# Kernel optimization log

Hardware: AMD Instinct MI355X
Metric: run time of the kernel (lower is better)

## Reference

```python
import jax, jax.numpy as jnp
import numpy as np

B, S, D = 2, 2048, 1024
H = 16
HD = D // H  # 64
EPS = 1e-5


def setup_inputs() -> dict:
    key = jax.random.key(0)
    ks = jax.random.split(key, 9)
    s = 1.0 / np.sqrt(D)
    return {
        "x": jax.random.normal(ks[0], (B, S, D), jnp.float32),
        "Wq": jax.random.normal(ks[1], (D, D), jnp.float32) * s,
        "bq": jnp.zeros((D,), jnp.float32),
        "Wk": jax.random.normal(ks[2], (D, D), jnp.float32) * s,
        "bk": jnp.zeros((D,), jnp.float32),
        "Wv": jax.random.normal(ks[3], (D, D), jnp.float32) * s,
        "bv": jnp.zeros((D,), jnp.float32),
        "Wp": jax.random.normal(ks[4], (D, D), jnp.float32) * s,
        "bp": jnp.zeros((D,), jnp.float32),
        "gamma": jnp.ones((D,), jnp.float32),
        "beta": jnp.zeros((D,), jnp.float32),
    }


def reference(x, Wq, bq, Wk, bk, Wv, bv, Wp, bp, gamma, beta):
    # QKV projections -> [B, H, S, HD]
    def split_heads(t):
        return t.reshape(B, S, H, HD).transpose(0, 2, 1, 3)

    q = split_heads(x @ Wq + bq)
    k = split_heads(x @ Wk + bk)
    v = split_heads(x @ Wv + bv)

    scores = jnp.einsum('bhqd,bhkd->bhqk', q, k) / np.sqrt(HD).astype(jnp.float32)
    attn = jax.nn.softmax(scores, axis=-1)  # dropout in eval mode = identity
    out = jnp.einsum('bhqk,bhkd->bhqd', attn, v)
    out = out.transpose(0, 2, 1, 3).reshape(B, S, D)
    out = out @ Wp + bp  # dropout identity

    # residual + LayerNorm over last dim
    y = x + out
    mu = jnp.mean(y, axis=-1, keepdims=True)
    var = jnp.mean((y - mu) ** 2, axis=-1, keepdims=True)
    return (y - mu) / jnp.sqrt(var + EPS) * gamma + beta
```

## Files before the change

kernel.cpp:

```cpp
#include <hip/hip_runtime.h>

#define DI __device__ __forceinline__

typedef __bf16 bf16;
typedef __bf16 bf16x8 __attribute__((ext_vector_type(8)));
typedef __bf16 bf16x4 __attribute__((ext_vector_type(4)));
typedef float  f32x4  __attribute__((ext_vector_type(4)));

DI void async_copy16(const void* g, void* s) {
  __builtin_amdgcn_global_load_lds(
      (__attribute__((address_space(1))) unsigned int*)(void*)g,
      (__attribute__((address_space(3))) unsigned int*)s,
      16, 0, 0);
}

DI f32x4 mfma16(bf16x8 a, bf16x8 b, f32x4 c) {
  return __builtin_amdgcn_mfma_f32_16x16x32_bf16(a, b, c, 0, 0, 0);
}


__global__ __launch_bounds__(256) void convert_x(const float* __restrict__ x,
                                                 bf16* __restrict__ xb) {
  int t = blockIdx.x * 256 + threadIdx.x;
  float4 v = ((const float4*)x)[t];
  bf16x4 o;
  o[0] = (bf16)v.x; o[1] = (bf16)v.y; o[2] = (bf16)v.z; o[3] = (bf16)v.w;
  *(bf16x4*)&xb[t * 4] = o;
}

__global__ __launch_bounds__(256) void transpose_w(const float* __restrict__ Wq,
                                                   const float* __restrict__ Wk,
                                                   const float* __restrict__ Wv,
                                                   const float* __restrict__ Wp,
                                                   bf16* __restrict__ Wt) {
  __shared__ float tile[32][33];
  const float* W = (blockIdx.z == 0) ? Wq : (blockIdx.z == 1) ? Wk
                 : (blockIdx.z == 2) ? Wv : Wp;
  int n0 = blockIdx.x * 32, k0 = blockIdx.y * 32;
  int tx = threadIdx.x, ty = threadIdx.y;
#pragma unroll
  for (int i = 0; i < 4; ++i)
    tile[ty + i * 8][tx] = W[(k0 + ty + i * 8) * 1024 + n0 + tx];
  __syncthreads();
#pragma unroll
  for (int i = 0; i < 4; ++i)
    Wt[((int)blockIdx.z * 1024 + n0 + ty + i * 8) * 1024 + k0 + tx] =
        (bf16)tile[tx][ty + i * 8];
}

template <int MODE, int MT, int NT>
__global__ __launch_bounds__(256, 3) void gemm_bt(
    const bf16* __restrict__ A, const bf16* __restrict__ Bt,
    const float* __restrict__ bias0, const float* __restrict__ bias1,
    const float* __restrict__ bias2, bf16* __restrict__ Qo,
    bf16* __restrict__ Ko, bf16* __restrict__ Vo, float* __restrict__ Po) {
  constexpr int MW = MT / 2, NW = NT / 2;
  constexpr int MI = MW / 16, NI = NW / 16;
  const int tid = threadIdx.x;
  const int w = tid >> 6, lane = tid & 63, quad = lane >> 4, m16 = lane & 15;
  const int m0 = blockIdx.x * MT, n0 = blockIdx.y * NT;
  const int mw = (w >> 1) * MW, nw = (w & 1) * NW;
  const int sw = m16 & 7;

  __shared__ __align__(16) bf16 As[MT * 64];
  __shared__ __align__(16) bf16 Bs[NT * 64];

  f32x4 acc[MI][NI];
#pragma unroll
  for (int i = 0; i < MI; ++i)
#pragma unroll
    for (int j = 0; j < NI; ++j)
#pragma unroll
      for (int r = 0; r < 4; ++r) acc[i][j][r] = 0.0f;

  for (int k0 = 0; k0 < 1024; k0 += 64) {
    __syncthreads();
#pragma unroll
    for (int i = 0; i < MT / 32; ++i) {
      int lin = i * 256 + tid;
      int row = lin >> 3, p = lin & 7;
      async_copy16(&A[(m0 + row) * 1024 + k0 + ((p ^ (row & 7)) << 3)],
                   &As[(i * 256 + w * 64) * 8]);
    }
#pragma unroll
    for (int i = 0; i < NT / 32; ++i) {
      int lin = i * 256 + tid;
      int row = lin >> 3, p = lin & 7;
      async_copy16(&Bt[(n0 + row) * 1024 + k0 + ((p ^ (row & 7)) << 3)],
                   &Bs[(i * 256 + w * 64) * 8]);
    }
    __syncthreads();

#pragma unroll
    for (int kk = 0; kk < 2; ++kk) {
      const int pos = ((kk * 4 + quad) ^ sw) << 3;
      bf16x8 af[MI], bg[NI];
#pragma unroll
      for (int i = 0; i < MI; ++i)
        af[i] = *(const bf16x8*)&As[(mw + i * 16 + m16) * 64 + pos];
#pragma unroll
      for (int j = 0; j < NI; ++j)
        bg[j] = *(const bf16x8*)&Bs[(nw + j * 16 + m16) * 64 + pos];
#pragma unroll
      for (int i = 0; i < MI; ++i)
#pragma unroll
        for (int j = 0; j < NI; ++j) acc[i][j] = mfma16(af[i], bg[j], acc[i][j]);
    }
  }

  const float SC = 0.18033688011112042f;
#pragma unroll
  for (int i = 0; i < MI; ++i) {
#pragma unroll
    for (int j = 0; j < NI; ++j) {
      int np = n0 + nw + j * 16 + m16;
      if (MODE == 0) {
        int which = np >> 10, n = np & 1023;
        float bias = (which == 0) ? bias0[n] : (which == 1) ? bias1[n] : bias2[n];
        int h = n >> 6, hd = n & 63;
        if (which == 2) {
          bf16x4 pv;
          int m = m0 + mw + i * 16 + quad * 4;
          int b = m >> 11, s = m & 2047;
#pragma unroll
          for (int r = 0; r < 4; ++r) pv[r] = (bf16)(acc[i][j][r] + bias);
          *(bf16x4*)&Vo[((b * 16 + h) * 64 + hd) * 2048 + s] = pv;
        } else {
#pragma unroll
          for (int r = 0; r < 4; ++r) {
            int m = m0 + mw + i * 16 + quad * 4 + r;
            int b = m >> 11, s = m & 2047;
            float v = acc[i][j][r] + bias;
            if (which == 0)
              Qo[((b * 16 + h) * 2048 + s) * 64 + hd] = (bf16)(v * SC);
            else
              Ko[((b * 16 + h) * 2048 + s) * 64 + hd] = (bf16)v;
          }
        }
      } else {
        float bias = bias0[np];
#pragma unroll
        for (int r = 0; r < 4; ++r) {
          int m = m0 + mw + i * 16 + quad * 4 + r;
          Po[m * 1024 + np] = acc[i][j][r] + bias;
        }
      }
    }
  }
}

__global__ __launch_bounds__(256, 2) void flash_kernel(const bf16* __restrict__ Q,
                                                       const bf16* __restrict__ K,
                                                       const bf16* __restrict__ Vt,
                                                       bf16* __restrict__ attn) {
  const int S = 2048;
  const int tid = threadIdx.x;
  const int w = tid >> 6, lane = tid & 63, quad = lane >> 4, m16 = lane & 15;
  const int bh = blockIdx.y, b = bh >> 4, h = bh & 15;
  const int qb = blockIdx.x * 128;
  const bf16* Qh = Q + bh * S * 64;
  const bf16* Kh = K + bh * S * 64;
  const bf16* Vh = Vt + bh * 64 * S;

  __shared__ __align__(16) bf16 Ks[64 * 64];
  __shared__ __align__(16) bf16 Vs[64 * 64];
  __shared__ __align__(16) bf16 Ps[4][16 * 72];

  bf16x8 qf[2][2];
#pragma unroll
  for (int mi = 0; mi < 2; ++mi)
#pragma unroll
    for (int kk = 0; kk < 2; ++kk)
      qf[mi][kk] = *(const bf16x8*)&Qh[(qb + w * 32 + mi * 16 + m16) * 64 +
                                       kk * 32 + quad * 8];

  bf16x8 ones;
#pragma unroll
  for (int j = 0; j < 8; ++j) ones[j] = (bf16)1.0f;

  f32x4 o[2][4];
  f32x4 lacc[2];
#pragma unroll
  for (int mi = 0; mi < 2; ++mi) {
#pragma unroll
    for (int dt = 0; dt < 4; ++dt)
#pragma unroll
      for (int r = 0; r < 4; ++r) o[mi][dt][r] = 0.0f;
#pragma unroll
    for (int r = 0; r < 4; ++r) lacc[mi][r] = 0.0f;
  }

  for (int kb = 0; kb < S; kb += 64) {
    __syncthreads();
#pragma unroll
    for (int i = 0; i < 2; ++i) {
      int lin = i * 256 + tid;
      int row = lin >> 3, g = lin & 7;
      async_copy16(&Kh[(kb + row) * 64 + ((g ^ (row & 7)) << 3)],
                   &Ks[(i * 256 + w * 64) * 8]);
      async_copy16(&Vh[row * 2048 + kb + ((g ^ (row & 7)) << 3)],
                   &Vs[(i * 256 + w * 64) * 8]);
    }
    __syncthreads();

    bf16x8 kf[4][2], vf[4][2];
#pragma unroll
    for (int nt = 0; nt < 4; ++nt)
#pragma unroll
      for (int kk = 0; kk < 2; ++kk) {
        int row = nt * 16 + m16;
        int pos = (kk * 4 + quad) ^ (row & 7);
        kf[nt][kk] = *(const bf16x8*)&Ks[row * 64 + pos * 8];
        vf[nt][kk] = *(const bf16x8*)&Vs[row * 64 + pos * 8];
      }

    bf16* Pw = &Ps[w][0];
#pragma unroll
    for (int mi = 0; mi < 2; ++mi) {
      f32x4 sacc[4];
#pragma unroll
      for (int nt = 0; nt < 4; ++nt)
#pragma unroll
        for (int r = 0; r < 4; ++r) sacc[nt][r] = 0.0f;
#pragma unroll
      for (int nt = 0; nt < 4; ++nt)
#pragma unroll
        for (int kk = 0; kk < 2; ++kk)
          sacc[nt] = mfma16(kf[nt][kk], qf[mi][kk], sacc[nt]);

#pragma unroll
      for (int nt = 0; nt < 4; ++nt) {
        bf16x4 p4;
#pragma unroll
        for (int r = 0; r < 4; ++r)
          p4[r] = (bf16)__builtin_amdgcn_exp2f(sacc[nt][r]);
        *(bf16x4*)&Pw[m16 * 72 + nt * 16 + quad * 4] = p4;
      }
      asm volatile("s_waitcnt lgkmcnt(0)" ::: "memory");

      bf16x8 pf[2];
#pragma unroll
      for (int kk = 0; kk < 2; ++kk)
        pf[kk] = *(const bf16x8*)&Pw[m16 * 72 + kk * 32 + quad * 8];

#pragma unroll
      for (int kk = 0; kk < 2; ++kk) lacc[mi] = mfma16(pf[kk], ones, lacc[mi]);

#pragma unroll
      for (int dt = 0; dt < 4; ++dt)
#pragma unroll
        for (int kk = 0; kk < 2; ++kk)
          o[mi][dt] = mfma16(pf[kk], vf[dt][kk], o[mi][dt]);
    }
  }

#pragma unroll
  for (int mi = 0; mi < 2; ++mi) {
    f32x4 inv;
#pragma unroll
    for (int r = 0; r < 4; ++r) inv[r] = 1.0f / lacc[mi][r];
#pragma unroll
    for (int dt = 0; dt < 4; ++dt)
#pragma unroll
      for (int r = 0; r < 4; ++r) {
        int s = qb + w * 32 + mi * 16 + quad * 4 + r;
        int col = h * 64 + dt * 16 + m16;
        attn[(b * 2048 + s) * 1024 + col] = (bf16)(o[mi][dt][r] * inv[r]);
      }
  }
}

__global__ __launch_bounds__(256) void ln_kernel(const float* __restrict__ x,
                                                 const float* __restrict__ pj,
                                                 const float* __restrict__ gamma,
                                                 const float* __restrict__ beta,
                                                 float* __restrict__ out) {
  int row = blockIdx.x, t = threadIdx.x;
  int base = row * 1024 + t * 4;
  float4 xv = *(const float4*)&x[base];
  float4 pv = *(const float4*)&pj[base];
  float y0 = xv.x + pv.x, y1 = xv.y + pv.y, y2 = xv.z + pv.z, y3 = xv.w + pv.w;
  float s = y0 + y1 + y2 + y3;
  float ss = y0 * y0 + y1 * y1 + y2 * y2 + y3 * y3;
  for (int m = 1; m < 64; m <<= 1) {
    s += __shfl_xor(s, m);
    ss += __shfl_xor(ss, m);
  }
  __shared__ float sred[8];
  int w = t >> 6;
  if ((t & 63) == 0) { sred[w * 2] = s; sred[w * 2 + 1] = ss; }
  __syncthreads();
  s = sred[0] + sred[2] + sred[4] + sred[6];
  ss = sred[1] + sred[3] + sred[5] + sred[7];
  float mean = s * (1.0f / 1024.0f);
  float var = ss * (1.0f / 1024.0f) - mean * mean;
  float rstd = rsqrtf(var + 1e-5f);
  float4 gv = *(const float4*)&gamma[t * 4];
  float4 bv = *(const float4*)&beta[t * 4];
  float4 ov;
  ov.x = (y0 - mean) * rstd * gv.x + bv.x;
  ov.y = (y1 - mean) * rstd * gv.y + bv.y;
  ov.z = (y2 - mean) * rstd * gv.z + bv.z;
  ov.w = (y3 - mean) * rstd * gv.w + bv.w;
  *(float4*)&out[base] = ov;
}


extern "C" void kernel_launch(void* const* d_in, const int* in_sizes, int n_in,
                              void* d_out, int out_size, void* d_ws, size_t ws_size,
                              hipStream_t stream) {
  const float* x = (const float*)d_in[0];
  const float* Wq = (const float*)d_in[1];
  const float* bq = (const float*)d_in[2];
  const float* Wk = (const float*)d_in[3];
  const float* bk = (const float*)d_in[4];
  const float* Wv = (const float*)d_in[5];
  const float* bv = (const float*)d_in[6];
  const float* Wp = (const float*)d_in[7];
  const float* bp = (const float*)d_in[8];
  const float* gamma = (const float*)d_in[9];
  const float* beta = (const float*)d_in[10];
  float* out = (float*)d_out;

  char* ws = (char*)d_ws;
  bf16* xb = (bf16*)(ws);
  bf16* Wtb = (bf16*)(ws + (8u << 20));
  bf16* Qb = (bf16*)(ws + (16u << 20));
  bf16* Kb = (bf16*)(ws + (24u << 20));
  bf16* Vtb = (bf16*)(ws + (32u << 20));
  float* proj = (float*)(ws + (16u << 20));
  bf16* attn = xb;

  convert_x<<<4096, 256, 0, stream>>>(x, xb);
  transpose_w<<<dim3(32, 32, 4), dim3(32, 8), 0, stream>>>(Wq, Wk, Wv, Wp, Wtb);
  gemm_bt<0, 128, 128><<<dim3(32, 24), 256, 0, stream>>>(
      xb, Wtb, bq, bk, bv, Qb, Kb, Vtb, nullptr);
  flash_kernel<<<dim3(16, 32), 256, 0, stream>>>(Qb, Kb, Vtb, attn);
  gemm_bt<1, 64, 128><<<dim3(64, 8), 256, 0, stream>>>(
      attn, Wtb + 3072 * 1024, bp, nullptr, nullptr, nullptr, nullptr, nullptr,
      proj);
  ln_kernel<<<4096, 256, 0, stream>>>(x, proj, gamma, beta, out);
}
```

Before: 195.2 us.

## Split flash attention across waves along key dimension with LDS reduction

The flash kernel now assigns each block 64 queries, and each of its four waves processes a different 32-key slice of each 128-key tile. Partial outputs and row sums are combined through a shared-memory tree reduction at the end. The K layout and swizzle are rearranged so the exp'd scores stay in registers as the MFMA A-operand, which removes the per-wave P round trip through LDS. The grid doubles and occupancy is hinted at 3 blocks per CU, in exchange for more accumulator registers and an extra cross-wave reduction with several barriers.

```diff
diff --git a/kernel.cpp b/kernel.cpp
--- a/kernel.cpp
+++ b/kernel.cpp
@@ -149,7 +149,7 @@
   }
 }
 
-__global__ __launch_bounds__(256, 2) void flash_kernel(const bf16* __restrict__ Q,
+__global__ __launch_bounds__(256, 3) void flash_kernel(const bf16* __restrict__ Q,
                                                        const bf16* __restrict__ K,
                                                        const bf16* __restrict__ Vt,
                                                        bf16* __restrict__ attn) {
@@ -157,116 +157,164 @@
   const int tid = threadIdx.x;
   const int w = tid >> 6, lane = tid & 63, quad = lane >> 4, m16 = lane & 15;
   const int bh = blockIdx.y, b = bh >> 4, h = bh & 15;
-  const int qb = blockIdx.x * 128;
+  const int qb = blockIdx.x * 64;
   const bf16* Qh = Q + bh * S * 64;
   const bf16* Kh = K + bh * S * 64;
   const bf16* Vh = Vt + bh * 64 * S;
 
-  __shared__ __align__(16) bf16 Ks[64 * 64];
-  __shared__ __align__(16) bf16 Vs[64 * 64];
-  __shared__ __align__(16) bf16 Ps[4][16 * 72];
-
-  bf16x8 qf[2][2];
-#pragma unroll
-  for (int mi = 0; mi < 2; ++mi)
+  __shared__ __align__(16) char smem[2 * 80 * 68 * 4];
+  bf16* Ks = (bf16*)smem;
+  bf16* Vs = (bf16*)(smem + 16384);
+  float* red0 = (float*)smem;
+  float* red1 = (float*)(smem + 80 * 68 * 4);
+
+  bf16x8 qf[4][2];
+#pragma unroll
+  for (int qt = 0; qt < 4; ++qt)
 #pragma unroll
     for (int kk = 0; kk < 2; ++kk)
-      qf[mi][kk] = *(const bf16x8*)&Qh[(qb + w * 32 + mi * 16 + m16) * 64 +
-                                       kk * 32 + quad * 8];
+      qf[qt][kk] = *(const bf16x8*)&Qh[(qb + qt * 16 + m16) * 64 + kk * 32 +
+                                       quad * 8];
 
   bf16x8 ones;
 #pragma unroll
   for (int j = 0; j < 8; ++j) ones[j] = (bf16)1.0f;
 
-  f32x4 o[2][4];
-  f32x4 lacc[2];
-#pragma unroll
-  for (int mi = 0; mi < 2; ++mi) {
+  f32x4 o[4][4];
+  f32x4 lacc[4];
+#pragma unroll
+  for (int qt = 0; qt < 4; ++qt) {
 #pragma unroll
     for (int dt = 0; dt < 4; ++dt)
 #pragma unroll
-      for (int r = 0; r < 4; ++r) o[mi][dt][r] = 0.0f;
-#pragma unroll
-    for (int r = 0; r < 4; ++r) lacc[mi][r] = 0.0f;
-  }
-
-  for (int kb = 0; kb < S; kb += 64) {
-    __syncthreads();
-#pragma unroll
-    for (int i = 0; i < 2; ++i) {
+      for (int r = 0; r < 4; ++r) o[qt][dt][r] = 0.0f;
+#pragma unroll
+    for (int r = 0; r < 4; ++r) lacc[qt][r] = 0.0f;
+  }
+
+  const int krow0 = w * 32 + ((m16 >> 2) << 3) + (m16 & 3);
+  const int skk = (m16 & 3) | (((m16 >> 2) & 1) << 2);
+
+  for (int t = 0; t < 16; ++t) {
+    const int kb = t * 128;
+#pragma unroll
+    for (int i = 0; i < 4; ++i) {
       int lin = i * 256 + tid;
       int row = lin >> 3, g = lin & 7;
-      async_copy16(&Kh[(kb + row) * 64 + ((g ^ (row & 7)) << 3)],
+      int sk = (row & 3) | (((row >> 3) & 1) << 2);
+      async_copy16(&Kh[(kb + row) * 64 + ((g ^ sk) << 3)],
                    &Ks[(i * 256 + w * 64) * 8]);
+    }
+#pragma unroll
+    for (int i = 0; i < 4; ++i) {
+      int lin = i * 256 + tid;
+      int row = lin >> 4, g = lin & 15;
       async_copy16(&Vh[row * 2048 + kb + ((g ^ (row & 7)) << 3)],
                    &Vs[(i * 256 + w * 64) * 8]);
     }
     __syncthreads();
 
-    bf16x8 kf[4][2], vf[4][2];
-#pragma unroll
-    for (int nt = 0; nt < 4; ++nt)
+    bf16x8 kf[2][2], vf[4];
+#pragma unroll
+    for (int sub = 0; sub < 2; ++sub)
 #pragma unroll
       for (int kk = 0; kk < 2; ++kk) {
-        int row = nt * 16 + m16;
-        int pos = (kk * 4 + quad) ^ (row & 7);
-        kf[nt][kk] = *(const bf16x8*)&Ks[row * 64 + pos * 8];
-        vf[nt][kk] = *(const bf16x8*)&Vs[row * 64 + pos * 8];
+        int row = krow0 + sub * 4;
+        int pos = (kk * 4 + quad) ^ skk;
+        kf[sub][kk] = *(const bf16x8*)&Ks[row * 64 + pos * 8];
       }
-
-    bf16* Pw = &Ps[w][0];
-#pragma unroll
-    for (int mi = 0; mi < 2; ++mi) {
-      f32x4 sacc[4];
-#pragma unroll
-      for (int nt = 0; nt < 4; ++nt)
-#pragma unroll
-        for (int r = 0; r < 4; ++r) sacc[nt][r] = 0.0f;
-#pragma unroll
-      for (int nt = 0; nt < 4; ++nt)
-#pragma unroll
-        for (int kk = 0; kk < 2; ++kk)
-          sacc[nt] = mfma16(kf[nt][kk], qf[mi][kk], sacc[nt]);
-
-#pragma unroll
-      for (int nt = 0; nt < 4; ++nt) {
-        bf16x4 p4;
+#pragma unroll
+    for (int dt = 0; dt < 4; ++dt) {
+      int d = dt * 16 + m16;
+      int p = (w * 4 + quad) ^ (d & 7);
+      vf[dt] = *(const bf16x8*)&Vs[d * 128 + p * 8];
+    }
+
+#pragma unroll
+    for (int qt = 0; qt < 4; ++qt) {
+      f32x4 s0 = {0.f, 0.f, 0.f, 0.f}, s1 = {0.f, 0.f, 0.f, 0.f};
+#pragma unroll
+      for (int kk = 0; kk < 2; ++kk) {
+        s0 = mfma16(kf[0][kk], qf[qt][kk], s0);
+        s1 = mfma16(kf[1][kk], qf[qt][kk], s1);
+      }
+      bf16x8 pf;
+#pragma unroll
+      for (int r = 0; r < 4; ++r) {
+        pf[r]     = (bf16)__builtin_amdgcn_exp2f(s0[r]);
+        pf[r + 4] = (bf16)__builtin_amdgcn_exp2f(s1[r]);
+      }
+      lacc[qt] = mfma16(pf, ones, lacc[qt]);
+#pragma unroll
+      for (int dt = 0; dt < 4; ++dt)
+        o[qt][dt] = mfma16(pf, vf[dt], o[qt][dt]);
+    }
+    __syncthreads();
+  }
+
+  auto wr = [&](float* R) {
+#pragma unroll
+    for (int qt = 0; qt < 4; ++qt) {
+#pragma unroll
+      for (int dt = 0; dt < 4; ++dt)
 #pragma unroll
         for (int r = 0; r < 4; ++r)
-          p4[r] = (bf16)__builtin_amdgcn_exp2f(sacc[nt][r]);
-        *(bf16x4*)&Pw[m16 * 72 + nt * 16 + quad * 4] = p4;
-      }
-      asm volatile("s_waitcnt lgkmcnt(0)" ::: "memory");
-
-      bf16x8 pf[2];
-#pragma unroll
-      for (int kk = 0; kk < 2; ++kk)
-        pf[kk] = *(const bf16x8*)&Pw[m16 * 72 + kk * 32 + quad * 8];
-
-#pragma unroll
-      for (int kk = 0; kk < 2; ++kk) lacc[mi] = mfma16(pf[kk], ones, lacc[mi]);
-
+          R[(qt * 16 + dt * 4 + r) * 68 + lane] = o[qt][dt][r];
+#pragma unroll
+      for (int r = 0; r < 4; ++r)
+        R[(64 + qt * 4 + r) * 68 + lane] = lacc[qt][r];
+    }
+  };
+  auto acc = [&](const float* R) {
+#pragma unroll
+    for (int qt = 0; qt < 4; ++qt) {
 #pragma unroll
       for (int dt = 0; dt < 4; ++dt)
 #pragma unroll
-        for (int kk = 0; kk < 2; ++kk)
-          o[mi][dt] = mfma16(pf[kk], vf[dt][kk], o[mi][dt]);
-    }
-  }
-
-#pragma unroll
-  for (int mi = 0; mi < 2; ++mi) {
-    f32x4 inv;
-#pragma unroll
-    for (int r = 0; r < 4; ++r) inv[r] = 1.0f / lacc[mi][r];
-#pragma unroll
-    for (int dt = 0; dt < 4; ++dt)
-#pragma unroll
-      for (int r = 0; r < 4; ++r) {
-        int s = qb + w * 32 + mi * 16 + quad * 4 + r;
-        int col = h * 64 + dt * 16 + m16;
-        attn[(b * 2048 + s) * 1024 + col] = (bf16)(o[mi][dt][r] * inv[r]);
-      }
+        for (int r = 0; r < 4; ++r)
+          o[qt][dt][r] += R[(qt * 16 + dt * 4 + r) * 68 + lane];
+#pragma unroll
+      for (int r = 0; r < 4; ++r)
+        lacc[qt][r] += R[(64 + qt * 4 + r) * 68 + lane];
+    }
+  };
+
+  if (w == 1) wr(red0);
+  if (w == 3) wr(red1);
+  __syncthreads();
+  if (w == 0) acc(red0);
+  if (w == 2) acc(red1);
+  __syncthreads();
+  if (w == 2) wr(red0);
+  __syncthreads();
+  if (w == 0) {
+    acc(red0);
+    wr(red0);
+  }
+  __syncthreads();
+
+  {
+    int qloc = lane >> 2, db = lane & 3;
+    int e = w * 16 + db * 4 + (qloc & 3);
+    const float* base = &red0[e * 68 + (qloc >> 2) * 16];
+    f32x4 v0 = *(const f32x4*)(base);
+    f32x4 v1 = *(const f32x4*)(base + 4);
+    f32x4 v2 = *(const f32x4*)(base + 8);
+    f32x4 v3 = *(const f32x4*)(base + 12);
+    float ls = red0[(64 + w * 4 + (qloc & 3)) * 68 + (qloc >> 2) * 16];
+    float inv = 1.0f / ls;
+    bf16x8 h0, h1;
+#pragma unroll
+    for (int j = 0; j < 4; ++j) {
+      h0[j] = (bf16)(v0[j] * inv);
+      h0[j + 4] = (bf16)(v1[j] * inv);
+      h1[j] = (bf16)(v2[j] * inv);
+      h1[j + 4] = (bf16)(v3[j] * inv);
+    }
+    int qg = qb + w * 16 + qloc;
+    bf16* dst = &attn[(b * 2048 + qg) * 1024 + h * 64 + db * 16];
+    *(bf16x8*)dst = h0;
+    *(bf16x8*)(dst + 8) = h1;
   }
 }
 
@@ -335,7 +383,7 @@
   transpose_w<<<dim3(32, 32, 4), dim3(32, 8), 0, stream>>>(Wq, Wk, Wv, Wp, Wtb);
   gemm_bt<0, 128, 128><<<dim3(32, 24), 256, 0, stream>>>(
       xb, Wtb, bq, bk, bv, Qb, Kb, Vtb, nullptr);
-  flash_kernel<<<dim3(16, 32), 256, 0, stream>>>(Qb, Kb, Vtb, attn);
+  flash_kernel<<<dim3(32, 32), 256, 0, stream>>>(Qb, Kb, Vtb, attn);
   gemm_bt<1, 64, 128><<<dim3(64, 8), 256, 0, stream>>>(
       attn, Wtb + 3072 * 1024, bp, nullptr, nullptr, nullptr, nullptr, nullptr,
       proj);
```

Result: slower. 230.2 us (+17.9%).
